# Optimization experiments

Measured on AMD Instinct MI355X. Metric: run time of the kernel, lower is better.

## Reference

```python
import jax, jax.numpy as jnp
import numpy as np

H = 64  # hidden size per direction


def _lstm_dir(x, w_ih, w_hh, b_ih, b_hh, reverse):
    """Single-direction LSTM over x: [B, T, D] -> [B, T, H]. PyTorch gate order i,f,g,o."""
    B = x.shape[0]
    # Precompute input projections for all timesteps at once: [B, T, 4H]
    xg = jnp.einsum('btd,gd->btg', x, w_ih) + b_ih + b_hh

    def step(carry, xt):
        h, c = carry
        g = xt + h @ w_hh.T                       # [B, 4H]
        i, f, gc, o = jnp.split(g, 4, axis=-1)
        c = jax.nn.sigmoid(f) * c + jax.nn.sigmoid(i) * jnp.tanh(gc)
        h = jax.nn.sigmoid(o) * jnp.tanh(c)
        return (h, c), h

    init = (jnp.zeros((B, H), x.dtype), jnp.zeros((B, H), x.dtype))
    _, hs = jax.lax.scan(step, init, jnp.swapaxes(xg, 0, 1), reverse=reverse)
    return jnp.swapaxes(hs, 0, 1)  # [B, T, H]


def _bilstm(x, layer_params):
    out = x
    for (wif, whf, bif, bhf, wir, whr, bir, bhr) in layer_params:
        fwd = _lstm_dir(out, wif, whf, bif, bhf, reverse=False)
        bwd = _lstm_dir(out, wir, whr, bir, bhr, reverse=True)
        out = jnp.concatenate([fwd, bwd], axis=-1)  # [B, T, 2H]
    return out


def setup_inputs() -> dict:
    key = jax.random.key(0)
    ks = jax.random.split(key, 20)
    B, T, D = 1024, 256, 5
    s = 1.0 / np.sqrt(H)  # PyTorch LSTM init bound
    u = lambda k, shape: jax.random.uniform(k, shape, jnp.float32, -s, s)
    inp = {"x": jax.random.normal(ks[0], (B, T, D), jnp.float32)}
    dims = [D, 2 * H]
    i = 1
    for l in range(2):
        d = dims[l]
        for suf in ("", "r"):
            inp[f"w_ih_l{l}{suf}"] = u(ks[i], (4 * H, d)); i += 1
            inp[f"w_hh_l{l}{suf}"] = u(ks[i], (4 * H, H)); i += 1
            inp[f"b_ih_l{l}{suf}"] = u(ks[i], (4 * H,)); i += 1
            inp[f"b_hh_l{l}{suf}"] = u(ks[i], (4 * H,)); i += 1
    inp["fc_w"] = u(ks[17], (1, 2 * H))
    inp["fc_b"] = u(ks[18], (1,))
    return inp


def reference(x, w_ih_l0, w_hh_l0, b_ih_l0, b_hh_l0,
              w_ih_l0r, w_hh_l0r, b_ih_l0r, b_hh_l0r,
              w_ih_l1, w_hh_l1, b_ih_l1, b_hh_l1,
              w_ih_l1r, w_hh_l1r, b_ih_l1r, b_hh_l1r,
              fc_w, fc_b):
    layer_params = [
        (w_ih_l0, w_hh_l0, b_ih_l0, b_hh_l0, w_ih_l0r, w_hh_l0r, b_ih_l0r, b_hh_l0r),
        (w_ih_l1, w_hh_l1, b_ih_l1, b_hh_l1, w_ih_l1r, w_hh_l1r, b_ih_l1r, b_hh_l1r),
    ]
    out = _bilstm(x, layer_params)       # [B, T, 2H]
    last = out[:, -1, :]                 # [B, 2H]
    return last @ fc_w.T + fc_b          # [B, 1]
```

## Files before the change

### kernel.cpp

```cpp
#include <hip/hip_runtime.h>
#include <hip/hip_bf16.h>

#define HH 64
#define TT 256
#define NB 1024
#define GG 256
#define DD0 5
#define DD1 128

typedef __attribute__((ext_vector_type(8))) short bf16x8;
typedef __attribute__((ext_vector_type(4))) float f32x4;
typedef __attribute__((ext_vector_type(4))) unsigned int u32x4;

#define MFMA16(a, b, c) __builtin_amdgcn_mfma_f32_16x16x32_bf16((a), (b), (c), 0, 0, 0)

__device__ __forceinline__ void barrier_lds() {
    asm volatile("s_waitcnt lgkmcnt(0)\n\ts_barrier" ::: "memory");
}

__device__ __forceinline__ float rcp_fast(float x) {
    float r;
    asm("v_rcp_f32 %0, %1" : "=v"(r) : "v"(x));
    return r;
}
__device__ __forceinline__ float sigf(float x) { return rcp_fast(1.0f + __expf(-x)); }
__device__ __forceinline__ float tanh_fast(float x) { return 2.0f * rcp_fast(1.0f + __expf(-2.0f * x)) - 1.0f; }

__device__ __forceinline__ float bf2f(short s) {
    unsigned int u = ((unsigned int)(unsigned short)s) << 16;
    return __builtin_bit_cast(float, u);
}
__device__ __forceinline__ short f2bf_rne(float x) {
    unsigned int u = __builtin_bit_cast(unsigned int, x);
    u += 0x7fffu + ((u >> 16) & 1u);
    return (short)(u >> 16);
}


__launch_bounds__(512, 1)
__global__ void lstm_l0(const float* __restrict__ x,
                        const float* __restrict__ w_ih_f, const float* __restrict__ w_hh_f,
                        const float* __restrict__ b_ih_f, const float* __restrict__ b_hh_f,
                        const float* __restrict__ w_ih_r, const float* __restrict__ w_hh_r,
                        const float* __restrict__ b_ih_r, const float* __restrict__ b_hh_r,
                        unsigned int* __restrict__ out0) {
    const int tid  = threadIdx.x;
    const int W    = tid >> 6;
    const int dir  = W >> 2;
    const int w    = W & 3;
    const int l    = tid & 63;
    const int col  = l & 15;
    const int rg   = l >> 4;
    const int row0 = blockIdx.x * 4;
    const int u    = w * 16 + col;

    const float* w_ih = dir ? w_ih_r : w_ih_f;
    const float* w_hh = dir ? w_hh_r : w_hh_f;
    const float* b_ih = dir ? b_ih_r : b_ih_f;
    const float* b_hh = dir ? b_hh_r : b_hh_f;

    __shared__ __align__(16) unsigned int xpk[4 * 2056];
    __shared__ __align__(16) short hsf2[2][2][4 * 144];

    for (int i = tid; i < 4 * TT; i += 512) {
        const int row = i >> 8, t = i & 255;
        const float* xs = x + ((size_t)(row0 + row) * TT + t) * DD0;
        unsigned int xh[5], xl[5];
#pragma unroll
        for (int d = 0; d < DD0; ++d) {
            const float v = xs[d];
            const short hi = f2bf_rne(v);
            xh[d] = (unsigned short)hi;
            xl[d] = (unsigned short)f2bf_rne(v - bf2f(hi));
        }
        unsigned int* o = &xpk[row * 2056 + t * 8];
        o[0] = xh[0] | (xh[1] << 16);
        o[1] = xh[2] | (xh[3] << 16);
        o[2] = xh[4] | (xl[0] << 16);
        o[3] = xl[1] | (xl[2] << 16);
        o[4] = xl[3] | (xl[4] << 16);
        o[5] = xh[0] | (xh[1] << 16);
        o[6] = xh[2] | (xh[3] << 16);
        o[7] = xh[4] | (0x3f80u << 16);
    }
    for (int i = tid; i < 2 * 2 * 4 * 144; i += 512) ((short*)hsf2)[i] = 0;

    bf16x8 whh_hi[4][2], whh_lo[4][2];
#pragma unroll
    for (int q = 0; q < 4; ++q) {
        const int gate = (w + 4 * q) * 16 + col;
#pragma unroll
        for (int ks = 0; ks < 2; ++ks) {
            const float* src = w_hh + gate * HH + ks * 32 + 8 * rg;
#pragma unroll
            for (int e = 0; e < 8; ++e) {
                float v = src[e];
                short h16 = f2bf_rne(v);
                whh_hi[q][ks][e] = h16;
                whh_lo[q][ks][e] = f2bf_rne(v - bf2f(h16));
            }
        }
    }
    bf16x8 wxb[4];
#pragma unroll
    for (int q = 0; q < 4; ++q) {
        const int gate = (w + 4 * q) * 16 + col;
        short whi[5], wlo[5];
#pragma unroll
        for (int d = 0; d < DD0; ++d) {
            float v = w_ih[gate * DD0 + d];
            whi[d] = f2bf_rne(v);
            wlo[d] = f2bf_rne(v - bf2f(whi[d]));
        }
        const float bbv = b_ih[gate] + b_hh[gate];
        const short bbh = f2bf_rne(bbv);
        const short bbl = f2bf_rne(bbv - bf2f(bbh));
        bf16x8 bs = {};
        if (rg == 0) {
            bs[0] = whi[0]; bs[1] = whi[1]; bs[2] = whi[2]; bs[3] = whi[3]; bs[4] = whi[4];
            bs[5] = whi[0]; bs[6] = whi[1]; bs[7] = whi[2];
        } else if (rg == 1) {
            bs[0] = whi[3]; bs[1] = whi[4];
            bs[2] = wlo[0]; bs[3] = wlo[1]; bs[4] = wlo[2]; bs[5] = wlo[3]; bs[6] = wlo[4];
            bs[7] = bbh;
        } else if (rg == 2) {
            bs[0] = bbl;
        }
        wxb[q] = bs;
    }

    bf16x8 xf = {};
    if (rg == 2) xf[0] = (short)0x3f80;

    const int t0 = dir ? (TT - 1) : 0;
    unsigned int* po = out0 + ((size_t)(row0 + rg) * TT + t0) * 128 + dir * 64 + u;
    const int pstep = dir ? -128 : 128;

    const int arow = col >> 2;
    float cc = 0.f;
    __syncthreads();

    for (int t = 0; t < TT; ++t) {
        const int tt  = dir ? (TT - 1 - t) : t;
        const int cur = t & 1, nxt = cur ^ 1;

        if (rg < 2)
            xf = __builtin_bit_cast(bf16x8, *(const u32x4*)&xpk[arow * 2056 + tt * 8 + rg * 4]);

        const short* hb = &hsf2[dir][cur][0];
        bf16x8 ah0 = *(const bf16x8*)&hb[arow * 144 +  0 + 8 * rg];
        bf16x8 ah1 = *(const bf16x8*)&hb[arow * 144 + 32 + 8 * rg];
        bf16x8 ah2 = *(const bf16x8*)&hb[arow * 144 + 64 + 8 * rg];
        bf16x8 ah3 = *(const bf16x8*)&hb[arow * 144 + 96 + 8 * rg];
        f32x4 acc[4];
#pragma unroll
        for (int q = 0; q < 4; ++q) {
            f32x4 p0 = {0.f, 0.f, 0.f, 0.f};
            f32x4 p1 = {0.f, 0.f, 0.f, 0.f};
            p0 = MFMA16(xf, wxb[q], p0);
            p1 = MFMA16(ah0, whh_hi[q][0], p1);
            p0 = MFMA16(ah1, whh_hi[q][1], p0);
            p1 = MFMA16(ah2, whh_hi[q][0], p1);
            p0 = MFMA16(ah3, whh_hi[q][1], p0);
            p1 = MFMA16(ah0, whh_lo[q][0], p1);
            p0 = MFMA16(ah1, whh_lo[q][1], p0);
            acc[q] = p0 + p1;
        }
        const float cn = sigf(acc[1][0]) * cc + sigf(acc[0][0]) * tanh_fast(acc[2][0]);
        const float hn = sigf(acc[3][0]) * tanh_fast(cn);
        cc = cn;
        const short hi16 = f2bf_rne(hn);
        const short lo16 = f2bf_rne(hn - bf2f(hi16));
        hsf2[dir][nxt][rg * 144 + u]      = hi16;
        hsf2[dir][nxt][rg * 144 + 64 + u] = lo16;
        *po = (unsigned int)(unsigned short)hi16 |
              ((unsigned int)(unsigned short)lo16 << 16);
        po += pstep;
        barrier_lds();
    }
}

__launch_bounds__(512, 1)
__global__ void lstm_l1_pc(const unsigned int* __restrict__ h0,
                           const float* __restrict__ w_ih, const float* __restrict__ w_hh,
                           const float* __restrict__ b_ih, const float* __restrict__ b_hh,
                           float* __restrict__ h_last) {
    const int tid  = threadIdx.x;
    const int W    = tid >> 6;
    const int l    = tid & 63;
    const int col  = l & 15;
    const int rg   = l >> 4;
    const int row0 = blockIdx.x * 4;

    __shared__ __align__(16) short hsf2[2][4 * 144];
    __shared__ __align__(16) float ihaccf[2 * 4 * 64 * 20];
    __shared__ __align__(16) short wflo_s[4 * 4 * 4 * 512];

    for (int i = tid; i < 2 * 4 * 144; i += 512) ((short*)hsf2)[i] = 0;

    if (W < 4) {
        const int m = W;
        bf16x8 wf_hi[4][4];
        float bbq[4];
#pragma unroll
        for (int q = 0; q < 4; ++q) {
            const int gate = (m + 4 * q) * 16 + col;
            bbq[q] = b_ih[gate] + b_hh[gate];
#pragma unroll
            for (int ks = 0; ks < 4; ++ks) {
                const float* src = w_ih + gate * DD1 + ks * 32 + 8 * rg;
                bf16x8 hi, lo;
#pragma unroll
                for (int e = 0; e < 8; ++e) {
                    float v = src[e];
                    short h16 = f2bf_rne(v);
                    hi[e] = h16;
                    lo[e] = f2bf_rne(v - bf2f(h16));
                }
                wf_hi[q][ks] = hi;
                *(bf16x8*)&wflo_s[(((m * 4 + q) * 4 + ks) * 64 + l) * 8] = lo;
            }
        }
        const int arr = col & 3, aj = col >> 2;
        const unsigned int* xsrc = h0 + ((size_t)(row0 + arr) * TT + aj) * 128 + 8 * rg;

        bf16x8 xA[8], xB[8];
        auto loadx = [&](int tbase, bf16x8 (&xr)[8]) {
            const unsigned int* p = xsrc + (size_t)tbase * 128;
#pragma unroll
            for (int ks = 0; ks < 4; ++ks) {
                const u32x4 a0 = *(const u32x4*)&p[ks * 32];
                const u32x4 a1 = *(const u32x4*)&p[ks * 32 + 4];
                u32x4 hw = {(a0[0] & 0xffffu) | (a0[1] << 16), (a0[2] & 0xffffu) | (a0[3] << 16),
                            (a1[0] & 0xffffu) | (a1[1] << 16), (a1[2] & 0xffffu) | (a1[3] << 16)};
                u32x4 lw = {(a0[0] >> 16) | (a0[1] & 0xffff0000u), (a0[2] >> 16) | (a0[3] & 0xffff0000u),
                            (a1[0] >> 16) | (a1[1] & 0xffff0000u), (a1[2] >> 16) | (a1[3] & 0xffff0000u)};
                xr[ks]     = __builtin_bit_cast(bf16x8, hw);
                xr[4 + ks] = __builtin_bit_cast(bf16x8, lw);
            }
        };
        auto ih_q = [&](int q, const bf16x8 (&xr)[8], int buf) {
            bf16x8 wl0 = *(const bf16x8*)&wflo_s[(((m * 4 + q) * 4 + 0) * 64 + l) * 8];
            bf16x8 wl1 = *(const bf16x8*)&wflo_s[(((m * 4 + q) * 4 + 1) * 64 + l) * 8];
            bf16x8 wl2 = *(const bf16x8*)&wflo_s[(((m * 4 + q) * 4 + 2) * 64 + l) * 8];
            bf16x8 wl3 = *(const bf16x8*)&wflo_s[(((m * 4 + q) * 4 + 3) * 64 + l) * 8];
            f32x4 a0 = {0.f, 0.f, 0.f, 0.f};
            f32x4 a1 = {0.f, 0.f, 0.f, 0.f};
            f32x4 a2 = {0.f, 0.f, 0.f, 0.f};
#pragma unroll
            for (int ks = 0; ks < 4; ++ks) a0 = MFMA16(xr[ks],     wf_hi[q][ks], a0);
#pragma unroll
            for (int ks = 0; ks < 4; ++ks) a1 = MFMA16(xr[4 + ks], wf_hi[q][ks], a1);
            a2 = MFMA16(xr[0], wl0, a2);
            a2 = MFMA16(xr[1], wl1, a2);
            a2 = MFMA16(xr[2], wl2, a2);
            a2 = MFMA16(xr[3], wl3, a2);
            f32x4 a = (a0 + a1) + a2;
            a += bbq[q];
            const int ug = m * 16 + col;
            *(f32x4*)&ihaccf[((buf * 4 + rg) * 64 + ug) * 20 + q * 4] = a;
        };

        loadx(0, xA);
        ih_q(0, xA, 0); ih_q(1, xA, 0); ih_q(2, xA, 0); ih_q(3, xA, 0);
        loadx(4, xB);
        __syncthreads();

        for (int tb = 0; tb < TT; tb += 8) {
            if (tb + 8 < TT) loadx(tb + 8, xA);
            ih_q(0, xB, 1); barrier_lds();
            ih_q(1, xB, 1); barrier_lds();
            ih_q(2, xB, 1); barrier_lds();
            ih_q(3, xB, 1); barrier_lds();
            if (tb + 12 < TT) loadx(tb + 12, xB);
            const bool doih = (tb + 8 < TT);
            if (doih) ih_q(0, xA, 0);
            barrier_lds();
            if (doih) ih_q(1, xA, 0);
            barrier_lds();
            if (doih) ih_q(2, xA, 0);
            barrier_lds();
            if (doih) ih_q(3, xA, 0);
            barrier_lds();
        }
    } else {
        const int w = W - 4;
        const int u = w * 16 + col;
        const int g = rg;
        const int arow = (l & 15) >> 2;

        bf16x8 whh_hi[4][2], whh_lo[4][2];
#pragma unroll
        for (int q = 0; q < 4; ++q) {
            const int gate = (w + 4 * q) * 16 + col;
#pragma unroll
            for (int ks = 0; ks < 2; ++ks) {
                const float* src = w_hh + gate * HH + ks * 32 + 8 * rg;
#pragma unroll
                for (int e = 0; e < 8; ++e) {
                    float v = src[e];
                    short h16 = f2bf_rne(v);
                    whh_hi[q][ks][e] = h16;
                    whh_lo[q][ks][e] = f2bf_rne(v - bf2f(h16));
                }
            }
        }

        float cc = 0.f;
        __syncthreads();

        auto step = [&](int t, int k) {
            const int cur = k & 1, nxt = cur ^ 1;
            const int j = k & 3, ib = k >> 2;
            const float* ibase = &ihaccf[((ib * 4 + j) * 64 + u) * 20 + g];
            const float iv0 = ibase[0], iv1 = ibase[4], iv2 = ibase[8], iv3 = ibase[12];
            const short* hb = &hsf2[cur][0];
            bf16x8 ah0 = *(const bf16x8*)&hb[arow * 144 +  0 + 8 * rg];
            bf16x8 ah1 = *(const bf16x8*)&hb[arow * 144 + 32 + 8 * rg];
            bf16x8 ah2 = *(const bf16x8*)&hb[arow * 144 + 64 + 8 * rg];
            bf16x8 ah3 = *(const bf16x8*)&hb[arow * 144 + 96 + 8 * rg];
            f32x4 acc[4];
#pragma unroll
            for (int q = 0; q < 4; ++q) {
                f32x4 p0 = {0.f, 0.f, 0.f, 0.f};
                f32x4 p1 = {0.f, 0.f, 0.f, 0.f};
                p0 = MFMA16(ah0, whh_hi[q][0], p0);
                p1 = MFMA16(ah1, whh_hi[q][1], p1);
                p0 = MFMA16(ah2, whh_hi[q][0], p0);
                p1 = MFMA16(ah3, whh_hi[q][1], p1);
                p0 = MFMA16(ah0, whh_lo[q][0], p0);
                p1 = MFMA16(ah1, whh_lo[q][1], p1);
                acc[q] = p0 + p1;
            }
            const float gi_ = acc[0][0] + iv0;
            const float gf_ = acc[1][0] + iv1;
            const float gg_ = acc[2][0] + iv2;
            const float go_ = acc[3][0] + iv3;
            const float cn = sigf(gf_) * cc + sigf(gi_) * tanh_fast(gg_);
            const float hn = sigf(go_) * tanh_fast(cn);
            cc = cn;
            const short hi16 = f2bf_rne(hn);
            hsf2[nxt][g * 144 + u]      = hi16;
            hsf2[nxt][g * 144 + 64 + u] = f2bf_rne(hn - bf2f(hi16));
            if (t == TT - 1) h_last[(size_t)(row0 + g) * HH + u] = hn;
            barrier_lds();
        };

        for (int tb = 0; tb < TT; tb += 8) {
#pragma unroll
            for (int k = 0; k < 8; ++k) step(tb + k, k);
        }
    }
}

__global__ void lstm_tail(const unsigned int* __restrict__ in0,
                          const float* __restrict__ h1f,
                          const float* __restrict__ w_ih_r,
                          const float* __restrict__ b_ih_r, const float* __restrict__ b_hh_r,
                          const float* __restrict__ fc_w, const float* __restrict__ fc_b,
                          float* __restrict__ out) {
    const int b   = blockIdx.x;
    const int tid = threadIdx.x;
    __shared__ __align__(16) float insl[DD1];
    __shared__ __align__(16) float hb[HH];
    __shared__ __align__(16) float gsh[256];

    if (tid < DD1) {
        const unsigned int v = in0[((size_t)b * TT + (TT - 1)) * 128 + tid];
        insl[tid] = bf2f((short)(v & 0xffffu)) + bf2f((short)(v >> 16));
    }
    __syncthreads();

    float a0 = b_ih_r[tid] + b_hh_r[tid], a1 = 0.f, a2 = 0.f, a3 = 0.f;
    const float4* in4 = (const float4*)insl;
#pragma unroll
    for (int kk = 0; kk < 32; ++kk) {
        float4 iv = in4[kk];
        float4 wv = *(const float4*)&w_ih_r[tid * DD1 + 4 * kk];
        a0 += wv.x * iv.x;
        a1 += wv.y * iv.y;
        a2 += wv.z * iv.z;
        a3 += wv.w * iv.w;
    }
    gsh[tid] = (a0 + a1) + (a2 + a3);
    __syncthreads();

    if (tid < HH) {
        const float gi = gsh[tid], gc = gsh[tid + 128], go = gsh[tid + 192];
        const float ccv = sigf(gi) * tanh_fast(gc);
        hb[tid] = sigf(go) * tanh_fast(ccv);
    }
    __syncthreads();

    if (tid < 64) {
        float p = fc_w[tid] * h1f[(size_t)b * HH + tid] + fc_w[HH + tid] * hb[tid];
#pragma unroll
        for (int off = 32; off; off >>= 1) p += __shfl_xor(p, off);
        if (tid == 0) out[b] = p + fc_b[0];
    }
}

extern "C" void kernel_launch(void* const* d_in, const int* in_sizes, int n_in,
                              void* d_out, int out_size, void* d_ws, size_t ws_size,
                              hipStream_t stream) {
    const float* x = (const float*)d_in[0];
    char* ws = (char*)d_ws;
    const size_t out0_b = (size_t)NB * TT * 128 * 4;

    unsigned int* out0 = (unsigned int*)ws;
    float* h1f = (float*)(ws + out0_b);

    lstm_l0<<<256, 512, 0, stream>>>(
        x, (const float*)d_in[1], (const float*)d_in[2], (const float*)d_in[3], (const float*)d_in[4],
        (const float*)d_in[5], (const float*)d_in[6], (const float*)d_in[7], (const float*)d_in[8], out0);
    lstm_l1_pc<<<256, 512, 0, stream>>>(
        out0, (const float*)d_in[9], (const float*)d_in[10], (const float*)d_in[11],
        (const float*)d_in[12], h1f);
    lstm_tail<<<1024, 256, 0, stream>>>(
        out0, h1f, (const float*)d_in[13], (const float*)d_in[15], (const float*)d_in[16],
        (const float*)d_in[17], (const float*)d_in[18], (float*)d_out);
}
```

Measured before the change: 374.4 us.

## Split layer-0 LSTM into per-direction 2-row blocks with global x prefetch

Result: slower. 576.0 us (+53.9%).

```diff
diff --git a/kernel.cpp b/kernel.cpp
--- a/kernel.cpp
+++ b/kernel.cpp
@@ -37,21 +37,42 @@
 }
 
 
-__launch_bounds__(512, 1)
-__global__ void lstm_l0(const float* __restrict__ x,
+__global__ void prep_xpk(const float* __restrict__ x, unsigned int* __restrict__ xpk) {
+    const int i = blockIdx.x * 256 + threadIdx.x;
+    const float* xs = x + (size_t)i * DD0;
+    unsigned int xh[5], xl[5];
+#pragma unroll
+    for (int d = 0; d < DD0; ++d) {
+        const float v = xs[d];
+        const short hi = f2bf_rne(v);
+        xh[d] = (unsigned short)hi;
+        xl[d] = (unsigned short)f2bf_rne(v - bf2f(hi));
+    }
+    unsigned int* o = xpk + (size_t)i * 8;
+    o[0] = xh[0] | (xh[1] << 16);
+    o[1] = xh[2] | (xh[3] << 16);
+    o[2] = xh[4] | (xl[0] << 16);
+    o[3] = xl[1] | (xl[2] << 16);
+    o[4] = xl[3] | (xl[4] << 16);
+    o[5] = xh[0] | (xh[1] << 16);
+    o[6] = xh[2] | (xh[3] << 16);
+    o[7] = xh[4] | (0x3f80u << 16);
+}
+
+__launch_bounds__(256, 1)
+__global__ void lstm_l0(const unsigned int* __restrict__ xpk,
                         const float* __restrict__ w_ih_f, const float* __restrict__ w_hh_f,
                         const float* __restrict__ b_ih_f, const float* __restrict__ b_hh_f,
                         const float* __restrict__ w_ih_r, const float* __restrict__ w_hh_r,
                         const float* __restrict__ b_ih_r, const float* __restrict__ b_hh_r,
                         unsigned int* __restrict__ out0) {
     const int tid  = threadIdx.x;
-    const int W    = tid >> 6;
-    const int dir  = W >> 2;
-    const int w    = W & 3;
+    const int w    = tid >> 6;
     const int l    = tid & 63;
     const int col  = l & 15;
     const int rg   = l >> 4;
-    const int row0 = blockIdx.x * 4;
+    const int dir  = blockIdx.x & 1;
+    const int row0 = (blockIdx.x >> 1) * 2;
     const int u    = w * 16 + col;
 
     const float* w_ih = dir ? w_ih_r : w_ih_f;
@@ -59,31 +80,9 @@
     const float* b_ih = dir ? b_ih_r : b_ih_f;
     const float* b_hh = dir ? b_hh_r : b_hh_f;
 
-    __shared__ __align__(16) unsigned int xpk[4 * 2056];
-    __shared__ __align__(16) short hsf2[2][2][4 * 144];
-
-    for (int i = tid; i < 4 * TT; i += 512) {
-        const int row = i >> 8, t = i & 255;
-        const float* xs = x + ((size_t)(row0 + row) * TT + t) * DD0;
-        unsigned int xh[5], xl[5];
-#pragma unroll
-        for (int d = 0; d < DD0; ++d) {
-            const float v = xs[d];
-            const short hi = f2bf_rne(v);
-            xh[d] = (unsigned short)hi;
-            xl[d] = (unsigned short)f2bf_rne(v - bf2f(hi));
-        }
-        unsigned int* o = &xpk[row * 2056 + t * 8];
-        o[0] = xh[0] | (xh[1] << 16);
-        o[1] = xh[2] | (xh[3] << 16);
-        o[2] = xh[4] | (xl[0] << 16);
-        o[3] = xl[1] | (xl[2] << 16);
-        o[4] = xl[3] | (xl[4] << 16);
-        o[5] = xh[0] | (xh[1] << 16);
-        o[6] = xh[2] | (xh[3] << 16);
-        o[7] = xh[4] | (0x3f80u << 16);
-    }
-    for (int i = tid; i < 2 * 2 * 4 * 144; i += 512) ((short*)hsf2)[i] = 0;
+    __shared__ __align__(16) short hsf2[2][2 * 144];
+
+    for (int i = tid; i < 2 * 2 * 144; i += 256) ((short*)hsf2)[i] = 0;
 
     bf16x8 whh_hi[4][2], whh_lo[4][2];
 #pragma unroll
@@ -132,51 +131,71 @@
     bf16x8 xf = {};
     if (rg == 2) xf[0] = (short)0x3f80;
 
+    const int arow = col >> 3;
+    const int grow = rg >> 1;
+    const bool wr  = (rg & 1) == 0;
+
+    const unsigned int* xsrc = xpk + ((size_t)(row0 + arow) * TT) * 8 + rg * 4;
+
     const int t0 = dir ? (TT - 1) : 0;
-    unsigned int* po = out0 + ((size_t)(row0 + rg) * TT + t0) * 128 + dir * 64 + u;
+    unsigned int* po = out0 + ((size_t)(row0 + grow) * TT + t0) * 128 + dir * 64 + u;
     const int pstep = dir ? -128 : 128;
 
-    const int arow = col >> 2;
+    u32x4 xbuf[4];
+#pragma unroll
+    for (int p = 0; p < 4; ++p) {
+        const int ttp = dir ? (TT - 1 - p) : p;
+        if (rg < 2) xbuf[p] = *(const u32x4*)&xsrc[(size_t)ttp * 8];
+    }
+
     float cc = 0.f;
     __syncthreads();
 
-    for (int t = 0; t < TT; ++t) {
-        const int tt  = dir ? (TT - 1 - t) : t;
-        const int cur = t & 1, nxt = cur ^ 1;
-
-        if (rg < 2)
-            xf = __builtin_bit_cast(bf16x8, *(const u32x4*)&xpk[arow * 2056 + tt * 8 + rg * 4]);
-
-        const short* hb = &hsf2[dir][cur][0];
-        bf16x8 ah0 = *(const bf16x8*)&hb[arow * 144 +  0 + 8 * rg];
-        bf16x8 ah1 = *(const bf16x8*)&hb[arow * 144 + 32 + 8 * rg];
-        bf16x8 ah2 = *(const bf16x8*)&hb[arow * 144 + 64 + 8 * rg];
-        bf16x8 ah3 = *(const bf16x8*)&hb[arow * 144 + 96 + 8 * rg];
-        f32x4 acc[4];
-#pragma unroll
-        for (int q = 0; q < 4; ++q) {
-            f32x4 p0 = {0.f, 0.f, 0.f, 0.f};
-            f32x4 p1 = {0.f, 0.f, 0.f, 0.f};
-            p0 = MFMA16(xf, wxb[q], p0);
-            p1 = MFMA16(ah0, whh_hi[q][0], p1);
-            p0 = MFMA16(ah1, whh_hi[q][1], p0);
-            p1 = MFMA16(ah2, whh_hi[q][0], p1);
-            p0 = MFMA16(ah3, whh_hi[q][1], p0);
-            p1 = MFMA16(ah0, whh_lo[q][0], p1);
-            p0 = MFMA16(ah1, whh_lo[q][1], p0);
-            acc[q] = p0 + p1;
-        }
-        const float cn = sigf(acc[1][0]) * cc + sigf(acc[0][0]) * tanh_fast(acc[2][0]);
-        const float hn = sigf(acc[3][0]) * tanh_fast(cn);
-        cc = cn;
-        const short hi16 = f2bf_rne(hn);
-        const short lo16 = f2bf_rne(hn - bf2f(hi16));
-        hsf2[dir][nxt][rg * 144 + u]      = hi16;
-        hsf2[dir][nxt][rg * 144 + 64 + u] = lo16;
-        *po = (unsigned int)(unsigned short)hi16 |
-              ((unsigned int)(unsigned short)lo16 << 16);
-        po += pstep;
-        barrier_lds();
+    for (int tb = 0; tb < TT; tb += 8) {
+#pragma unroll
+        for (int k = 0; k < 8; ++k) {
+            const int t   = tb + k;
+            const int cur = t & 1, nxt = cur ^ 1;
+
+            if (rg < 2) xf = __builtin_bit_cast(bf16x8, xbuf[k & 3]);
+            if (rg < 2 && t + 4 < TT) {
+                const int ttn = dir ? (TT - 1 - (t + 4)) : (t + 4);
+                xbuf[k & 3] = *(const u32x4*)&xsrc[(size_t)ttn * 8];
+            }
+
+            const short* hb = &hsf2[cur][0];
+            bf16x8 ah0 = *(const bf16x8*)&hb[arow * 144 +  0 + 8 * rg];
+            bf16x8 ah1 = *(const bf16x8*)&hb[arow * 144 + 32 + 8 * rg];
+            bf16x8 ah2 = *(const bf16x8*)&hb[arow * 144 + 64 + 8 * rg];
+            bf16x8 ah3 = *(const bf16x8*)&hb[arow * 144 + 96 + 8 * rg];
+            f32x4 acc[4];
+#pragma unroll
+            for (int q = 0; q < 4; ++q) {
+                f32x4 p0 = {0.f, 0.f, 0.f, 0.f};
+                f32x4 p1 = {0.f, 0.f, 0.f, 0.f};
+                p0 = MFMA16(xf, wxb[q], p0);
+                p1 = MFMA16(ah0, whh_hi[q][0], p1);
+                p0 = MFMA16(ah1, whh_hi[q][1], p0);
+                p1 = MFMA16(ah2, whh_hi[q][0], p1);
+                p0 = MFMA16(ah3, whh_hi[q][1], p0);
+                p1 = MFMA16(ah0, whh_lo[q][0], p1);
+                p0 = MFMA16(ah1, whh_lo[q][1], p0);
+                acc[q] = p0 + p1;
+            }
+            const float cn = sigf(acc[1][0]) * cc + sigf(acc[0][0]) * tanh_fast(acc[2][0]);
+            const float hn = sigf(acc[3][0]) * tanh_fast(cn);
+            cc = cn;
+            const short hi16 = f2bf_rne(hn);
+            const short lo16 = f2bf_rne(hn - bf2f(hi16));
+            if (wr) {
+                hsf2[nxt][grow * 144 + u]      = hi16;
+                hsf2[nxt][grow * 144 + 64 + u] = lo16;
+                *po = (unsigned int)(unsigned short)hi16 |
+                      ((unsigned int)(unsigned short)lo16 << 16);
+            }
+            po += pstep;
+            barrier_lds();
+        }
     }
 }
 
@@ -406,12 +425,15 @@
     const float* x = (const float*)d_in[0];
     char* ws = (char*)d_ws;
     const size_t out0_b = (size_t)NB * TT * 128 * 4;
-
-    unsigned int* out0 = (unsigned int*)ws;
-    float* h1f = (float*)(ws + out0_b);
-
-    lstm_l0<<<256, 512, 0, stream>>>(
-        x, (const float*)d_in[1], (const float*)d_in[2], (const float*)d_in[3], (const float*)d_in[4],
+    const size_t h1f_b  = (size_t)NB * HH * 4;
+
+    unsigned int* out0  = (unsigned int*)ws;
+    float* h1f          = (float*)(ws + out0_b);
+    unsigned int* xpk   = (unsigned int*)(ws + out0_b + h1f_b);
+
+    prep_xpk<<<NB * TT / 256, 256, 0, stream>>>(x, xpk);
+    lstm_l0<<<1024, 256, 0, stream>>>(
+        xpk, (const float*)d_in[1], (const float*)d_in[2], (const float*)d_in[3], (const float*)d_in[4],
         (const float*)d_in[5], (const float*)d_in[6], (const float*)d_in[7], (const float*)d_in[8], out0);
     lstm_l1_pc<<<256, 512, 0, stream>>>(
         out0, (const float*)d_in[9], (const float*)d_in[10], (const float*)d_in[11],
```
